# Kernel optimization log

Measured on AMD Instinct MI355X. Metric: run time of the kernel, lower is better.

The kernel has to match this reference:

```python
import jax, jax.numpy as jnp
import numpy as np

B, T, P, E = 4, 16, 256, 768
H, D = 12, 64          # num_heads, kq_size; H*D == E
DFF = 3072
SCALE = D ** (-0.5)
EPS = 1e-5


def _ln(x, g, b):
    m = jnp.mean(x, axis=-1, keepdims=True)
    v = jnp.mean((x - m) ** 2, axis=-1, keepdims=True)
    return (x - m) / jnp.sqrt(v + EPS) * g + b


def setup_inputs() -> dict:
    key = jax.random.key(0)
    ks = jax.random.split(key, 16)
    std = 0.02
    d = {"x": jax.random.normal(ks[0], (B, T, P, E), jnp.float32)}
    # spatial attention params (weights stored as (in, out))
    d["sq_w"] = jax.random.normal(ks[1], (E, H * D), jnp.float32) * std
    d["sk_w"] = jax.random.normal(ks[2], (E, H * D), jnp.float32) * std
    d["sv_w"] = jax.random.normal(ks[3], (E, H * D), jnp.float32) * std
    d["so_w"] = jax.random.normal(ks[4], (H * D, E), jnp.float32) * std
    d["sq_b"] = jnp.zeros((H * D,), jnp.float32)
    d["sk_b"] = jnp.zeros((H * D,), jnp.float32)
    d["sv_b"] = jnp.zeros((H * D,), jnp.float32)
    d["so_b"] = jnp.zeros((E,), jnp.float32)
    d["sg"] = jnp.ones((E,), jnp.float32)
    d["sb"] = jnp.zeros((E,), jnp.float32)
    # temporal attention params
    d["tq_w"] = jax.random.normal(ks[5], (E, H * D), jnp.float32) * std
    d["tk_w"] = jax.random.normal(ks[6], (E, H * D), jnp.float32) * std
    d["tv_w"] = jax.random.normal(ks[7], (E, H * D), jnp.float32) * std
    d["to_w"] = jax.random.normal(ks[8], (H * D, E), jnp.float32) * std
    d["tq_b"] = jnp.zeros((H * D,), jnp.float32)
    d["tk_b"] = jnp.zeros((H * D,), jnp.float32)
    d["tv_b"] = jnp.zeros((H * D,), jnp.float32)
    d["to_b"] = jnp.zeros((E,), jnp.float32)
    d["tg"] = jnp.ones((E,), jnp.float32)
    d["tb"] = jnp.zeros((E,), jnp.float32)
    # FFN + final layernorm
    d["w1"] = jax.random.normal(ks[9], (E, DFF), jnp.float32) * std
    d["b1"] = jnp.zeros((DFF,), jnp.float32)
    d["w2"] = jax.random.normal(ks[10], (DFF, E), jnp.float32) * std
    d["b2"] = jnp.zeros((E,), jnp.float32)
    d["g"] = jnp.ones((E,), jnp.float32)
    d["bb"] = jnp.zeros((E,), jnp.float32)
    return d


def reference(x, sq_w, sq_b, sk_w, sk_b, sv_w, sv_b, so_w, so_b, sg, sb,
              tq_w, tq_b, tk_w, tk_b, tv_w, tv_b, to_w, to_b, tg, tb,
              w1, b1, w2, b2, g, bb):
    b, t, p, e = x.shape

    # ---- Spatial layer: attention over patches P within each frame ----
    q = (x @ sq_w + sq_b).reshape(b, t, p, H, D)
    k = (x @ sk_w + sk_b).reshape(b, t, p, H, D)
    v = (x @ sv_w + sv_b).reshape(b, t, p, H, D)
    attn = jnp.einsum('btphd,btqhd->bthpq', q, k) * SCALE
    attn = jax.nn.softmax(attn, axis=-1)
    out = jnp.einsum('bthpq,btqhd->btphd', attn, v).reshape(b, t, p, H * D)
    out = out @ so_w + so_b
    x = _ln(x + out, sg, sb)

    # ---- Temporal layer: causal attention over frames T per patch ----
    q = (x @ tq_w + tq_b).reshape(b, t, p, H, D)
    k = (x @ tk_w + tk_b).reshape(b, t, p, H, D)
    v = (x @ tv_w + tv_b).reshape(b, t, p, H, D)
    attn = jnp.einsum('btphd,bsphd->bphts', q, k) * SCALE
    causal = jnp.where(jnp.arange(t)[:, None] >= jnp.arange(t)[None, :],
                       jnp.float32(0), -jnp.inf).astype(x.dtype)  # (T, T)
    attn = attn + causal
    attn = jax.nn.softmax(attn, axis=-1)
    out = jnp.einsum('bphts,bsphd->btphd', attn, v).reshape(b, t, p, H * D)
    out = out @ to_w + to_b
    x = _ln(x + out, tg, tb)

    # ---- Feed forward + final layernorm ----
    ff = jax.nn.gelu(x @ w1 + b1, approximate=False) @ w2 + b2
    x = _ln(x + ff, g, bb)
    return x
```

## Files before the change

### kernel.cpp

```cpp
#include <hip/hip_runtime.h>
#include <math.h>

constexpr int cB   = 4;
constexpr int cT   = 16;
constexpr int cP   = 256;
constexpr int cE   = 768;
constexpr int cH   = 12;
constexpr int cD   = 64;
constexpr int cDFF = 3072;
constexpr int NTOK = cB * cT * cP;
constexpr float cSCALE = 0.125f;
constexpr float cEPS = 1e-5f;

typedef __attribute__((ext_vector_type(8))) short short8;
typedef __attribute__((ext_vector_type(4))) float f32x4;
typedef __attribute__((ext_vector_type(8))) unsigned short u16x8;
typedef __attribute__((ext_vector_type(4))) unsigned short u16x4;

#define AS1 __attribute__((address_space(1)))
#define AS3 __attribute__((address_space(3)))

__device__ inline float b2f(unsigned short u) {
    union { unsigned int i; float f; } c; c.i = ((unsigned int)u) << 16; return c.f;
}
__device__ inline unsigned short f2b(float f) {
    union { float f; unsigned int i; } c; c.f = f;
    unsigned int i = c.i;
    unsigned int r = i + 0x7FFFu + ((i >> 16) & 1u);
    return (unsigned short)(r >> 16);
}

__device__ inline void gload16(const unsigned short* g, short* l) {
    __builtin_amdgcn_global_load_lds((AS1 const void*)g, (AS3 void*)l, 16, 0, 0);
}

template<int OUTB, int ACT>
__global__ __launch_bounds__(256) void gemm_mfma_kernel(
    const unsigned short* __restrict__ A,
    const unsigned short* __restrict__ BT,
    const float* __restrict__ bias,
    void* __restrict__ Cout,
    int M, int N, int K)
{
    __shared__ short As[8192];
    __shared__ short Bs[8192];

    const int tid = threadIdx.x;
    const int m0 = blockIdx.y * 128;
    const int n0 = blockIdx.x * 128;
    const int w  = tid >> 6;
    const int l  = tid & 63;
    const int wr = w >> 1, wc = w & 1;
    const int l15 = l & 15, l16 = l >> 4;

    f32x4 acc[4][4];
    #pragma unroll
    for (int i = 0; i < 4; ++i)
        #pragma unroll
        for (int j = 0; j < 4; ++j)
            #pragma unroll
            for (int r = 0; r < 4; ++r) acc[i][j][r] = 0.f;

    const int sr = tid >> 2;
    const int sc = (tid & 3) << 3;
    const unsigned short* ga0 = A  + (size_t)(m0 + sr) * K + sc;
    const unsigned short* ga1 = A  + (size_t)(m0 + 64 + sr) * K + sc;
    const unsigned short* gb0 = BT + (size_t)(n0 + sr) * K + sc;
    const unsigned short* gb1 = BT + (size_t)(n0 + 64 + sr) * K + sc;
    short* lA = As + tid * 8;
    short* lB = Bs + tid * 8;

    const int aoff = (wr * 64 + l15) * 32 + l16 * 8;
    const int boff = (wc * 64 + l15) * 32 + l16 * 8;

    gload16(ga0, lA);
    gload16(ga1, lA + 2048);
    gload16(gb0, lB);
    gload16(gb1, lB + 2048);
    __syncthreads();

    int cur = 0;
    for (int k0 = 0; k0 < K; k0 += 32) {
        if (k0 + 32 < K) {
            const int nb = (cur ^ 1) << 12;
            gload16(ga0 + k0 + 32, lA + nb);
            gload16(ga1 + k0 + 32, lA + nb + 2048);
            gload16(gb0 + k0 + 32, lB + nb);
            gload16(gb1 + k0 + 32, lB + nb + 2048);
        }
        const int cb = cur << 12;
        short8 aF[4], bF[4];
        #pragma unroll
        for (int mf = 0; mf < 4; ++mf)
            aF[mf] = *(const short8*)(As + cb + aoff + mf * 512);
        #pragma unroll
        for (int nf = 0; nf < 4; ++nf)
            bF[nf] = *(const short8*)(Bs + cb + boff + nf * 512);
        #pragma unroll
        for (int mf = 0; mf < 4; ++mf)
            #pragma unroll
            for (int nf = 0; nf < 4; ++nf)
                acc[mf][nf] = __builtin_amdgcn_mfma_f32_16x16x32_bf16(
                    aF[mf], bF[nf], acc[mf][nf], 0, 0, 0);
        __syncthreads();
        cur ^= 1;
    }

    #pragma unroll
    for (int mf = 0; mf < 4; ++mf) {
        #pragma unroll
        for (int nf = 0; nf < 4; ++nf) {
            const int col = n0 + wc * 64 + nf * 16 + l15;
            const float bs = bias[col];
            #pragma unroll
            for (int r = 0; r < 4; ++r) {
                const int row = m0 + wr * 64 + mf * 16 + l16 * 4 + r;
                float v = acc[mf][nf][r] + bs;
                if (ACT) v = 0.5f * v * (1.f + erff(v * 0.70710678118654752f));
                if (OUTB) ((unsigned short*)Cout)[(size_t)row * N + col] = f2b(v);
                else      ((float*)Cout)[(size_t)row * N + col] = v;
            }
        }
    }
}

__global__ __launch_bounds__(256) void transpose_cast_kernel(
    const float* __restrict__ W, unsigned short* __restrict__ WT,
    int K, int N)
{
    __shared__ float t[32][33];
    const int k0 = blockIdx.y * 32;
    const int n0 = blockIdx.x * 32;
    const int tx = threadIdx.x & 31;
    const int ty4 = (threadIdx.x >> 5) << 2;
    #pragma unroll
    for (int i = 0; i < 4; ++i)
        t[ty4 + i][tx] = W[(size_t)(k0 + ty4 + i) * N + n0 + tx];
    __syncthreads();
    #pragma unroll
    for (int i = 0; i < 4; ++i)
        WT[(size_t)(n0 + ty4 + i) * K + k0 + tx] = f2b(t[tx][ty4 + i]);
}

struct TP8 { const float* src[8]; unsigned short* dst[8]; };
__global__ __launch_bounds__(256) void transpose_cast8_kernel(TP8 p)
{
    __shared__ float t[32][33];
    const int z = blockIdx.z;
    const float* W = p.src[z];
    unsigned short* WT = p.dst[z];
    const int k0 = blockIdx.y * 32;
    const int n0 = blockIdx.x * 32;
    const int tx = threadIdx.x & 31;
    const int ty4 = (threadIdx.x >> 5) << 2;
    #pragma unroll
    for (int i = 0; i < 4; ++i)
        t[ty4 + i][tx] = W[(size_t)(k0 + ty4 + i) * cE + n0 + tx];
    __syncthreads();
    #pragma unroll
    for (int i = 0; i < 4; ++i)
        WT[(size_t)(n0 + ty4 + i) * cE + k0 + tx] = f2b(t[tx][ty4 + i]);
}

__global__ __launch_bounds__(256) void cast_bf16_kernel(
    const float* __restrict__ in, unsigned short* __restrict__ out, int n4)
{
    for (int i = blockIdx.x * blockDim.x + threadIdx.x; i < n4;
         i += gridDim.x * blockDim.x) {
        float4 v = ((const float4*)in)[i];
        u16x4 o;
        o[0] = f2b(v.x); o[1] = f2b(v.y); o[2] = f2b(v.z); o[3] = f2b(v.w);
        *(u16x4*)(out + (size_t)i * 4) = o;
    }
}

__global__ __launch_bounds__(256) void residual_ln_kernel(
    const float* __restrict__ X, const float* __restrict__ R,
    const float* __restrict__ gamma, const float* __restrict__ beta,
    float* __restrict__ out, unsigned short* __restrict__ outb)
{
    const int row = blockIdx.x;
    const size_t off = (size_t)row * cE;
    const int tid = threadIdx.x;

    float v[3];
    float s = 0.f, ss = 0.f;
    #pragma unroll
    for (int i = 0; i < 3; ++i) {
        const int e = tid + i * 256;
        const float t = X[off + e] + R[off + e];
        v[i] = t; s += t; ss += t * t;
    }
    #pragma unroll
    for (int o = 32; o > 0; o >>= 1) {
        s  += __shfl_down(s, o);
        ss += __shfl_down(ss, o);
    }
    __shared__ float rs[4], rss[4];
    const int wid = tid >> 6;
    if ((tid & 63) == 0) { rs[wid] = s; rss[wid] = ss; }
    __syncthreads();
    s  = rs[0] + rs[1] + rs[2] + rs[3];
    ss = rss[0] + rss[1] + rss[2] + rss[3];

    const float mean = s * (1.f / cE);
    const float var  = ss * (1.f / cE) - mean * mean;
    const float inv  = rsqrtf(var + cEPS);
    #pragma unroll
    for (int i = 0; i < 3; ++i) {
        const int e = tid + i * 256;
        const float r = (v[i] - mean) * inv * gamma[e] + beta[e];
        out[off + e] = r;
        if (outb) outb[off + e] = f2b(r);
    }
}

__global__ __launch_bounds__(256) void spatial_attn_mfma_kernel(
    const unsigned short* __restrict__ Q, const unsigned short* __restrict__ K,
    const unsigned short* __restrict__ V, unsigned short* __restrict__ O)
{
    __shared__ short Ks[64 * 64];
    __shared__ short Vt[64 * 64];
    __shared__ short Ps[4][64 * 64];

    const int bid = blockIdx.x;
    const int h  = bid % cH;
    const int bt = bid / cH;
    const size_t base = (size_t)bt * cP * cE + h * cD;

    const int tid = threadIdx.x;
    const int w = tid >> 6, l = tid & 63;
    const int l15 = l & 15, l16 = l >> 4;

    short8 qf[4][2];
    #pragma unroll
    for (int mf = 0; mf < 4; ++mf)
        #pragma unroll
        for (int kf = 0; kf < 2; ++kf)
            qf[mf][kf] = *(const short8*)(
                Q + base + (size_t)(w * 64 + mf * 16 + l15) * cE + kf * 32 + l16 * 8);

    f32x4 o[4][4];
    float mrun[4][4], lrun[4][4];
    #pragma unroll
    for (int mf = 0; mf < 4; ++mf)
        #pragma unroll
        for (int j = 0; j < 4; ++j) {
            #pragma unroll
            for (int r = 0; r < 4; ++r) o[mf][j][r] = 0.f;
            mrun[mf][j] = -INFINITY; lrun[mf][j] = 0.f;
        }

    const int krow = w * 8 + (l >> 3);
    const int kc16 = l & 7;
    const int vj  = tid & 31;
    const int vd0 = (tid >> 5) * 8;

    for (int c0 = 0; c0 < cP; c0 += 64) {
        __syncthreads();
        #pragma unroll
        for (int p = 0; p < 2; ++p) {
            const int row = p * 32 + krow;
            gload16(K + base + (size_t)(c0 + row) * cE + ((kc16 ^ (row & 7)) << 3),
                    Ks + row * 64 + kc16 * 8);
        }
        #pragma unroll
        for (int p = 0; p < 2; ++p) {
            const int j = p * 32 + vj;
            short8 vv = *(const short8*)(V + base + (size_t)(c0 + j) * cE + vd0);
            char* vb = (char*)Vt;
            #pragma unroll
            for (int e = 0; e < 8; ++e) {
                const int row = vd0 + e;
                *(short*)(vb + row * 128 + ((2 * j) ^ ((row & 7) << 4))) = vv[e];
            }
        }
        __syncthreads();

        f32x4 s[4][4];
        #pragma unroll
        for (int mf = 0; mf < 4; ++mf)
            #pragma unroll
            for (int nf = 0; nf < 4; ++nf)
                #pragma unroll
                for (int r = 0; r < 4; ++r) s[mf][nf][r] = 0.f;

        #pragma unroll
        for (int nf = 0; nf < 4; ++nf) {
            const int row = nf * 16 + l15;
            const char* kb = (const char*)Ks + row * 128;
            const int sw = (row & 7) << 4;
            short8 k0 = *(const short8*)(kb + ((l16 * 16) ^ sw));
            short8 k1 = *(const short8*)(kb + ((64 + l16 * 16) ^ sw));
            #pragma unroll
            for (int mf = 0; mf < 4; ++mf) {
                s[mf][nf] = __builtin_amdgcn_mfma_f32_16x16x32_bf16(qf[mf][0], k0, s[mf][nf], 0, 0, 0);
                s[mf][nf] = __builtin_amdgcn_mfma_f32_16x16x32_bf16(qf[mf][1], k1, s[mf][nf], 0, 0, 0);
            }
        }

        #pragma unroll
        for (int mf = 0; mf < 4; ++mf)
            #pragma unroll
            for (int nf = 0; nf < 4; ++nf)
                #pragma unroll
                for (int r = 0; r < 4; ++r) s[mf][nf][r] *= cSCALE;

        #pragma unroll
        for (int mf = 0; mf < 4; ++mf) {
            #pragma unroll
            for (int r = 0; r < 4; ++r) {
                float rv = fmaxf(fmaxf(s[mf][0][r], s[mf][1][r]),
                                 fmaxf(s[mf][2][r], s[mf][3][r]));
                rv = fmaxf(rv, __shfl_xor(rv, 1));
                rv = fmaxf(rv, __shfl_xor(rv, 2));
                rv = fmaxf(rv, __shfl_xor(rv, 4));
                rv = fmaxf(rv, __shfl_xor(rv, 8));
                const float mn = fmaxf(mrun[mf][r], rv);
                const float al = __expf(mrun[mf][r] - mn);
                mrun[mf][r] = mn;
                float ps = 0.f;
                #pragma unroll
                for (int nf = 0; nf < 4; ++nf) {
                    const float pe = __expf(s[mf][nf][r] - mn);
                    s[mf][nf][r] = pe;
                    ps += pe;
                }
                ps += __shfl_xor(ps, 1);
                ps += __shfl_xor(ps, 2);
                ps += __shfl_xor(ps, 4);
                ps += __shfl_xor(ps, 8);
                lrun[mf][r] = lrun[mf][r] * al + ps;
                #pragma unroll
                for (int df = 0; df < 4; ++df) o[mf][df][r] *= al;
            }
        }

        char* pw = (char*)&Ps[w][0];
        #pragma unroll
        for (int mf = 0; mf < 4; ++mf)
            #pragma unroll
            for (int nf = 0; nf < 4; ++nf)
                #pragma unroll
                for (int r = 0; r < 4; ++r) {
                    const int row = mf * 16 + l16 * 4 + r;
                    *(short*)(pw + row * 128 + (((nf * 16 + l15) * 2) ^ ((row & 7) << 4))) =
                        (short)f2b(s[mf][nf][r]);
                }

        short8 pa[4][2];
        #pragma unroll
        for (int mf = 0; mf < 4; ++mf) {
            const int prow = mf * 16 + l15;
            const char* pb = (const char*)&Ps[w][0] + prow * 128;
            const int sw = (prow & 7) << 4;
            pa[mf][0] = *(const short8*)(pb + ((l16 * 16) ^ sw));
            pa[mf][1] = *(const short8*)(pb + ((64 + l16 * 16) ^ sw));
        }
        #pragma unroll
        for (int df = 0; df < 4; ++df) {
            const int vrow = df * 16 + l15;
            const char* vbb = (const char*)Vt + vrow * 128;
            const int sw = (vrow & 7) << 4;
            short8 v0 = *(const short8*)(vbb + ((l16 * 16) ^ sw));
            short8 v1 = *(const short8*)(vbb + ((64 + l16 * 16) ^ sw));
            #pragma unroll
            for (int mf = 0; mf < 4; ++mf) {
                o[mf][df] = __builtin_amdgcn_mfma_f32_16x16x32_bf16(pa[mf][0], v0, o[mf][df], 0, 0, 0);
                o[mf][df] = __builtin_amdgcn_mfma_f32_16x16x32_bf16(pa[mf][1], v1, o[mf][df], 0, 0, 0);
            }
        }
    }

    #pragma unroll
    for (int mf = 0; mf < 4; ++mf)
        #pragma unroll
        for (int r = 0; r < 4; ++r) {
            const float inv = 1.f / lrun[mf][r];
            const size_t rowoff = base + (size_t)(w * 64 + mf * 16 + l16 * 4 + r) * cE;
            #pragma unroll
            for (int df = 0; df < 4; ++df)
                O[rowoff + df * 16 + l15] = f2b(o[mf][df][r] * inv);
        }
}

__global__ __launch_bounds__(128) void temporal_attn_kernel(
    const unsigned short* __restrict__ Q, const unsigned short* __restrict__ Kb,
    const unsigned short* __restrict__ V, unsigned short* __restrict__ O)
{
    const int bid = blockIdx.x;
    const int hg  = bid & 1;
    const int bp  = bid >> 1;
    const int p   = bp % cP;
    const int b   = bp / cP;

    __shared__ float Ks[cT][6][cD + 1];
    __shared__ float Vs[cT][6][cD + 1];

    const size_t framestride = (size_t)cP * cE;
    const size_t base0 = ((size_t)(b * cT) * cP + p) * cE + hg * 384;

    for (int li = threadIdx.x; li < cT * 384; li += 128) {
        const int s = li / 384;
        const int r = li % 384;
        const size_t src = base0 + (size_t)s * framestride + r;
        Ks[s][r / 64][r & 63] = b2f(Kb[src]);
        Vs[s][r / 64][r & 63] = b2f(V[src]);
    }
    __syncthreads();
    if (threadIdx.x >= 96) return;

    const int hh = threadIdx.x >> 4;
    const int t  = threadIdx.x & 15;
    const size_t qoff = ((size_t)(b * cT + t) * cP + p) * cE + hg * 384 + hh * cD;

    float q[cD];
    #pragma unroll
    for (int d = 0; d < cD; d += 8) {
        short8 f = *(const short8*)(Q + qoff + d);
        #pragma unroll
        for (int j = 0; j < 8; ++j) q[d + j] = b2f((unsigned short)f[j]);
    }

    float sc[cT];
    float mx = -INFINITY;
    #pragma unroll
    for (int s = 0; s < cT; ++s) {
        float acc = 0.f;
        #pragma unroll
        for (int d = 0; d < cD; ++d) acc = fmaf(q[d], Ks[s][hh][d], acc);
        sc[s] = (s <= t) ? acc * cSCALE : -INFINITY;
        mx = fmaxf(mx, sc[s]);
    }
    float l = 0.f;
    #pragma unroll
    for (int s = 0; s < cT; ++s) {
        const float e_ = __expf(sc[s] - mx);
        sc[s] = e_;
        l += e_;
    }
    float o[cD];
    #pragma unroll
    for (int d = 0; d < cD; ++d) o[d] = 0.f;
    #pragma unroll
    for (int s = 0; s < cT; ++s) {
        const float pj = sc[s];
        #pragma unroll
        for (int d = 0; d < cD; ++d) o[d] = fmaf(pj, Vs[s][hh][d], o[d]);
    }
    const float invl = 1.f / l;
    unsigned short* op = O + qoff;
    #pragma unroll
    for (int d = 0; d < cD; d += 8) {
        u16x8 f;
        #pragma unroll
        for (int j = 0; j < 8; ++j) f[j] = f2b(o[d + j] * invl);
        *(u16x8*)(op + d) = f;
    }
}

extern "C" void kernel_launch(void* const* d_in, const int* in_sizes, int n_in,
                              void* d_out, int out_size, void* d_ws, size_t ws_size,
                              hipStream_t stream)
{
    const float* x    = (const float*)d_in[0];
    const float* sq_w = (const float*)d_in[1];
    const float* sk_w = (const float*)d_in[2];
    const float* sv_w = (const float*)d_in[3];
    const float* so_w = (const float*)d_in[4];
    const float* sq_b = (const float*)d_in[5];
    const float* sk_b = (const float*)d_in[6];
    const float* sv_b = (const float*)d_in[7];
    const float* so_b = (const float*)d_in[8];
    const float* sg   = (const float*)d_in[9];
    const float* sb   = (const float*)d_in[10];
    const float* tq_w = (const float*)d_in[11];
    const float* tk_w = (const float*)d_in[12];
    const float* tv_w = (const float*)d_in[13];
    const float* to_w = (const float*)d_in[14];
    const float* tq_b = (const float*)d_in[15];
    const float* tk_b = (const float*)d_in[16];
    const float* tv_b = (const float*)d_in[17];
    const float* to_b = (const float*)d_in[18];
    const float* tg   = (const float*)d_in[19];
    const float* tb   = (const float*)d_in[20];
    const float* w1   = (const float*)d_in[21];
    const float* b1   = (const float*)d_in[22];
    const float* w2   = (const float*)d_in[23];
    const float* b2   = (const float*)d_in[24];
    const float* g    = (const float*)d_in[25];
    const float* bb   = (const float*)d_in[26];

    const size_t NE = (size_t)NTOK * cE;
    const size_t EE = (size_t)cE * cE;

    float* W0 = (float*)d_ws;
    float* Wp = W0 + NE;
    unsigned short* Xb = (unsigned short*)(Wp + NE);
    unsigned short* Qb = Xb + NE;
    unsigned short* Kbuf = Qb + NE;
    unsigned short* Vb = Kbuf + NE;
    unsigned short* Ob = Vb + NE;
    unsigned short* Hb = Qb;
    unsigned short* WT = Ob + NE;
    unsigned short* sqT = WT;
    unsigned short* skT = sqT + EE;
    unsigned short* svT = skT + EE;
    unsigned short* soT = svT + EE;
    unsigned short* tqT = soT + EE;
    unsigned short* tkT = tqT + EE;
    unsigned short* tvT = tkT + EE;
    unsigned short* toT = tvT + EE;
    unsigned short* w1T = toT + EE;
    unsigned short* w2T = w1T + (size_t)cDFF * cE;

    const dim3 blk(256);
    const dim3 gLN(NTOK);
    const dim3 gProj(cE / 128, NTOK / 128);
    const dim3 gFF1(cDFF / 128, NTOK / 128);

    cast_bf16_kernel<<<dim3(2048), blk, 0, stream>>>(x, Xb, (int)(NE / 4));
    {
        TP8 p;
        p.src[0] = sq_w; p.dst[0] = sqT;
        p.src[1] = sk_w; p.dst[1] = skT;
        p.src[2] = sv_w; p.dst[2] = svT;
        p.src[3] = so_w; p.dst[3] = soT;
        p.src[4] = tq_w; p.dst[4] = tqT;
        p.src[5] = tk_w; p.dst[5] = tkT;
        p.src[6] = tv_w; p.dst[6] = tvT;
        p.src[7] = to_w; p.dst[7] = toT;
        transpose_cast8_kernel<<<dim3(cE / 32, cE / 32, 8), blk, 0, stream>>>(p);
    }
    transpose_cast_kernel<<<dim3(cDFF / 32, cE / 32), blk, 0, stream>>>(w1, w1T, cE, cDFF);
    transpose_cast_kernel<<<dim3(cE / 32, cDFF / 32), blk, 0, stream>>>(w2, w2T, cDFF, cE);

    gemm_mfma_kernel<1,0><<<gProj, blk, 0, stream>>>(Xb, sqT, sq_b, Qb, NTOK, cE, cE);
    gemm_mfma_kernel<1,0><<<gProj, blk, 0, stream>>>(Xb, skT, sk_b, Kbuf, NTOK, cE, cE);
    gemm_mfma_kernel<1,0><<<gProj, blk, 0, stream>>>(Xb, svT, sv_b, Vb, NTOK, cE, cE);
    spatial_attn_mfma_kernel<<<dim3(cB * cT * cH), blk, 0, stream>>>(Qb, Kbuf, Vb, Ob);
    gemm_mfma_kernel<0,0><<<gProj, blk, 0, stream>>>(Ob, soT, so_b, Wp, NTOK, cE, cE);
    residual_ln_kernel<<<gLN, blk, 0, stream>>>(x, Wp, sg, sb, W0, Xb);

    gemm_mfma_kernel<1,0><<<gProj, blk, 0, stream>>>(Xb, tqT, tq_b, Qb, NTOK, cE, cE);
    gemm_mfma_kernel<1,0><<<gProj, blk, 0, stream>>>(Xb, tkT, tk_b, Kbuf, NTOK, cE, cE);
    gemm_mfma_kernel<1,0><<<gProj, blk, 0, stream>>>(Xb, tvT, tv_b, Vb, NTOK, cE, cE);
    temporal_attn_kernel<<<dim3(cB * cP * 2), dim3(128), 0, stream>>>(Qb, Kbuf, Vb, Ob);
    gemm_mfma_kernel<0,0><<<gProj, blk, 0, stream>>>(Ob, toT, to_b, Wp, NTOK, cE, cE);
    residual_ln_kernel<<<gLN, blk, 0, stream>>>(W0, Wp, tg, tb, W0, Xb);

    gemm_mfma_kernel<1,1><<<gFF1, blk, 0, stream>>>(Xb, w1T, b1, Hb, NTOK, cDFF, cE);
    gemm_mfma_kernel<0,0><<<gProj, blk, 0, stream>>>(Hb, w2T, b2, Wp, NTOK, cE, cDFF);
    residual_ln_kernel<<<gLN, blk, 0, stream>>>(W0, Wp, g, bb, (float*)d_out, nullptr);
}
```

Baseline: 785.8 us.

## Replace GEMM with 256x256 swizzled-LDS pipelined kernel and fuse QKV projections

```diff
diff --git a/kernel.cpp b/kernel.cpp
--- a/kernel.cpp
+++ b/kernel.cpp
@@ -34,91 +34,143 @@
     __builtin_amdgcn_global_load_lds((AS1 const void*)g, (AS3 void*)l, 16, 0, 0);
 }
 
-template<int OUTB, int ACT>
-__global__ __launch_bounds__(256) void gemm_mfma_kernel(
+__device__ inline void stage_half(const unsigned short* Xg, int K,
+                                  short* ldsbase, int w, int l) {
+    #pragma unroll
+    for (int j = 0; j < 2; ++j) {
+        const int r = w * 16 + j * 8 + (l >> 3);
+        const int sl = l & 7;
+        gload16(Xg + (size_t)r * K + ((sl ^ (r & 7)) << 3),
+                ldsbase + r * 64 + (sl << 3));
+    }
+}
+
+template<int OUTB, int ACT, int SPLIT3>
+__global__ __launch_bounds__(512, 2) void gemm256_kernel(
     const unsigned short* __restrict__ A,
     const unsigned short* __restrict__ BT,
-    const float* __restrict__ bias,
-    void* __restrict__ Cout,
-    int M, int N, int K)
-{
-    __shared__ short As[8192];
-    __shared__ short Bs[8192];
+    const float* __restrict__ bias0, const float* __restrict__ bias1,
+    const float* __restrict__ bias2,
+    void* __restrict__ C0, void* __restrict__ C1, void* __restrict__ C2,
+    int M, int N, int K, int nbn)
+{
+    __shared__ short As[2 * 256 * 64];
+    __shared__ short Bs[2 * 256 * 64];
 
     const int tid = threadIdx.x;
-    const int m0 = blockIdx.y * 128;
-    const int n0 = blockIdx.x * 128;
-    const int w  = tid >> 6;
-    const int l  = tid & 63;
-    const int wr = w >> 1, wc = w & 1;
+    const int w = tid >> 6, l = tid & 63;
     const int l15 = l & 15, l16 = l >> 4;
-
-    f32x4 acc[4][4];
-    #pragma unroll
-    for (int i = 0; i < 4; ++i)
+    const int wm = w >> 2, wn = w & 3;
+
+    const int nwg = gridDim.x;
+    const int wg = (blockIdx.x & 7) * (nwg >> 3) + (blockIdx.x >> 3);
+    const int bm = wg / nbn, bn = wg % nbn;
+    const int m0 = bm * 256, n0 = bn * 256;
+
+    const unsigned short* pA0 = A + (size_t)m0 * K;
+    const unsigned short* pA1 = A + (size_t)(m0 + 128) * K;
+    const unsigned short* pB0 = BT + (size_t)n0 * K;
+    const unsigned short* pB1 = BT + (size_t)(n0 + 128) * K;
+
+    f32x4 acc[8][4];
+    #pragma unroll
+    for (int i = 0; i < 8; ++i)
         #pragma unroll
         for (int j = 0; j < 4; ++j)
             #pragma unroll
             for (int r = 0; r < 4; ++r) acc[i][j][r] = 0.f;
 
-    const int sr = tid >> 2;
-    const int sc = (tid & 3) << 3;
-    const unsigned short* ga0 = A  + (size_t)(m0 + sr) * K + sc;
-    const unsigned short* ga1 = A  + (size_t)(m0 + 64 + sr) * K + sc;
-    const unsigned short* gb0 = BT + (size_t)(n0 + sr) * K + sc;
-    const unsigned short* gb1 = BT + (size_t)(n0 + 64 + sr) * K + sc;
-    short* lA = As + tid * 8;
-    short* lB = Bs + tid * 8;
-
-    const int aoff = (wr * 64 + l15) * 32 + l16 * 8;
-    const int boff = (wc * 64 + l15) * 32 + l16 * 8;
-
-    gload16(ga0, lA);
-    gload16(ga1, lA + 2048);
-    gload16(gb0, lB);
-    gload16(gb1, lB + 2048);
-    __syncthreads();
-
-    int cur = 0;
-    for (int k0 = 0; k0 < K; k0 += 32) {
-        if (k0 + 32 < K) {
-            const int nb = (cur ^ 1) << 12;
-            gload16(ga0 + k0 + 32, lA + nb);
-            gload16(ga1 + k0 + 32, lA + nb + 2048);
-            gload16(gb0 + k0 + 32, lB + nb);
-            gload16(gb1 + k0 + 32, lB + nb + 2048);
-        }
-        const int cb = cur << 12;
-        short8 aF[4], bF[4];
-        #pragma unroll
-        for (int mf = 0; mf < 4; ++mf)
-            aF[mf] = *(const short8*)(As + cb + aoff + mf * 512);
-        #pragma unroll
-        for (int nf = 0; nf < 4; ++nf)
-            bF[nf] = *(const short8*)(Bs + cb + boff + nf * 512);
-        #pragma unroll
-        for (int mf = 0; mf < 4; ++mf)
-            #pragma unroll
-            for (int nf = 0; nf < 4; ++nf)
-                acc[mf][nf] = __builtin_amdgcn_mfma_f32_16x16x32_bf16(
-                    aF[mf], bF[nf], acc[mf][nf], 0, 0, 0);
-        __syncthreads();
-        cur ^= 1;
-    }
-
-    #pragma unroll
-    for (int mf = 0; mf < 4; ++mf) {
+    stage_half(pA0, K, As, w, l);
+    stage_half(pA1, K, As + 8192, w, l);
+    stage_half(pB0, K, Bs, w, l);
+    stage_half(pB1, K, Bs + 8192, w, l);
+    asm volatile("s_waitcnt vmcnt(0)" ::: "memory");
+    __builtin_amdgcn_s_barrier();
+
+    short8 bF[4][2];
+    const int niter = K >> 7;
+    int k0 = 0;
+    for (int it = 0; it < niter; ++it) {
+        const int kb = k0 + 64;
+        const int kc = (k0 + 128 < K) ? (k0 + 128) : 0;
+        #pragma unroll
+        for (int p = 0; p < 8; ++p) {
+            const int c = p >> 2;
+            const int q = p & 3;
+
+            short8 aF[2][2];
+            if (q == 0) {
+                #pragma unroll
+                for (int nf = 0; nf < 4; ++nf) {
+                    const int rb = wn * 64 + nf * 16 + l15;
+                    const char* pb = (const char*)Bs + c * 32768 + rb * 128;
+                    const int sw = (rb & 7) << 4;
+                    bF[nf][0] = *(const short8*)(pb + ((l16 * 16) ^ sw));
+                    bF[nf][1] = *(const short8*)(pb + ((64 + l16 * 16) ^ sw));
+                }
+            }
+            #pragma unroll
+            for (int mm = 0; mm < 2; ++mm) {
+                const int ra = wm * 128 + (q * 2 + mm) * 16 + l15;
+                const char* pa = (const char*)As + c * 32768 + ra * 128;
+                const int sw = (ra & 7) << 4;
+                aF[mm][0] = *(const short8*)(pa + ((l16 * 16) ^ sw));
+                aF[mm][1] = *(const short8*)(pa + ((64 + l16 * 16) ^ sw));
+            }
+
+            {
+                const int koff = (p < 4) ? kb : kc;
+                short* dst = ((q < 2) ? As : Bs) + ((c ^ 1) * 16384) + ((q & 1) * 8192);
+                const unsigned short* src =
+                    (q == 0 ? pA0 : q == 1 ? pA1 : q == 2 ? pB0 : pB1) + koff;
+                stage_half(src, K, dst, w, l);
+            }
+
+            __builtin_amdgcn_s_barrier();
+            asm volatile("s_waitcnt lgkmcnt(0)" ::: "memory");
+            __builtin_amdgcn_sched_barrier(0);
+            __builtin_amdgcn_s_setprio(1);
+            #pragma unroll
+            for (int kk = 0; kk < 2; ++kk)
+                #pragma unroll
+                for (int nf = 0; nf < 4; ++nf)
+                    #pragma unroll
+                    for (int mm = 0; mm < 2; ++mm)
+                        acc[q * 2 + mm][nf] = __builtin_amdgcn_mfma_f32_16x16x32_bf16(
+                            aF[mm][kk], bF[nf][kk], acc[q * 2 + mm][nf], 0, 0, 0);
+            __builtin_amdgcn_s_setprio(0);
+            __builtin_amdgcn_sched_barrier(0);
+            if (q == 3)
+                asm volatile("s_waitcnt vmcnt(0)" ::: "memory");
+            __builtin_amdgcn_s_barrier();
+        }
+        k0 += 128;
+    }
+
+    #pragma unroll
+    for (int mf = 0; mf < 8; ++mf) {
         #pragma unroll
         for (int nf = 0; nf < 4; ++nf) {
-            const int col = n0 + wc * 64 + nf * 16 + l15;
-            const float bs = bias[col];
+            const int ng = n0 + wn * 64 + nf * 16 + l15;
+            int nl = ng;
+            const float* bp = bias0;
+            void* Cp = C0;
+            int Nout = N;
+            if (SPLIT3) {
+                const int which = ng / 768;
+                nl = ng - which * 768;
+                bp = (which == 0) ? bias0 : (which == 1) ? bias1 : bias2;
+                Cp = (which == 0) ? C0 : (which == 1) ? C1 : C2;
+                Nout = 768;
+            }
+            const float bs = bp[nl];
             #pragma unroll
             for (int r = 0; r < 4; ++r) {
-                const int row = m0 + wr * 64 + mf * 16 + l16 * 4 + r;
+                const int row = m0 + wm * 128 + mf * 16 + l16 * 4 + r;
                 float v = acc[mf][nf][r] + bs;
                 if (ACT) v = 0.5f * v * (1.f + erff(v * 0.70710678118654752f));
-                if (OUTB) ((unsigned short*)Cout)[(size_t)row * N + col] = f2b(v);
-                else      ((float*)Cout)[(size_t)row * N + col] = v;
+                if (OUTB) ((unsigned short*)Cp)[(size_t)row * Nout + nl] = f2b(v);
+                else      ((float*)Cp)[(size_t)row * Nout + nl] = v;
             }
         }
     }
@@ -515,9 +567,11 @@
     unsigned short* w2T = w1T + (size_t)cDFF * cE;
 
     const dim3 blk(256);
+    const dim3 blk512(512);
     const dim3 gLN(NTOK);
-    const dim3 gProj(cE / 128, NTOK / 128);
-    const dim3 gFF1(cDFF / 128, NTOK / 128);
+    const dim3 gQKV(576);
+    const dim3 gOUT(192);
+    const dim3 gFF1(768);
 
     cast_bf16_kernel<<<dim3(2048), blk, 0, stream>>>(x, Xb, (int)(NE / 4));
     {
@@ -535,21 +589,23 @@
     transpose_cast_kernel<<<dim3(cDFF / 32, cE / 32), blk, 0, stream>>>(w1, w1T, cE, cDFF);
     transpose_cast_kernel<<<dim3(cE / 32, cDFF / 32), blk, 0, stream>>>(w2, w2T, cDFF, cE);
 
-    gemm_mfma_kernel<1,0><<<gProj, blk, 0, stream>>>(Xb, sqT, sq_b, Qb, NTOK, cE, cE);
-    gemm_mfma_kernel<1,0><<<gProj, blk, 0, stream>>>(Xb, skT, sk_b, Kbuf, NTOK, cE, cE);
-    gemm_mfma_kernel<1,0><<<gProj, blk, 0, stream>>>(Xb, svT, sv_b, Vb, NTOK, cE, cE);
+    gemm256_kernel<1,0,1><<<gQKV, blk512, 0, stream>>>(
+        Xb, sqT, sq_b, sk_b, sv_b, Qb, Kbuf, Vb, NTOK, 2304, cE, 9);
     spatial_attn_mfma_kernel<<<dim3(cB * cT * cH), blk, 0, stream>>>(Qb, Kbuf, Vb, Ob);
-    gemm_mfma_kernel<0,0><<<gProj, blk, 0, stream>>>(Ob, soT, so_b, Wp, NTOK, cE, cE);
+    gemm256_kernel<0,0,0><<<gOUT, blk512, 0, stream>>>(
+        Ob, soT, so_b, nullptr, nullptr, Wp, nullptr, nullptr, NTOK, cE, cE, 3);
     residual_ln_kernel<<<gLN, blk, 0, stream>>>(x, Wp, sg, sb, W0, Xb);
 
-    gemm_mfma_kernel<1,0><<<gProj, blk, 0, stream>>>(Xb, tqT, tq_b, Qb, NTOK, cE, cE);
-    gemm_mfma_kernel<1,0><<<gProj, blk, 0, stream>>>(Xb, tkT, tk_b, Kbuf, NTOK, cE, cE);
-    gemm_mfma_kernel<1,0><<<gProj, blk, 0, stream>>>(Xb, tvT, tv_b, Vb, NTOK, cE, cE);
+    gemm256_kernel<1,0,1><<<gQKV, blk512, 0, stream>>>(
+        Xb, tqT, tq_b, tk_b, tv_b, Qb, Kbuf, Vb, NTOK, 2304, cE, 9);
     temporal_attn_kernel<<<dim3(cB * cP * 2), dim3(128), 0, stream>>>(Qb, Kbuf, Vb, Ob);
-    gemm_mfma_kernel<0,0><<<gProj, blk, 0, stream>>>(Ob, toT, to_b, Wp, NTOK, cE, cE);
+    gemm256_kernel<0,0,0><<<gOUT, blk512, 0, stream>>>(
+        Ob, toT, to_b, nullptr, nullptr, Wp, nullptr, nullptr, NTOK, cE, cE, 3);
     residual_ln_kernel<<<gLN, blk, 0, stream>>>(W0, Wp, tg, tb, W0, Xb);
 
-    gemm_mfma_kernel<1,1><<<gFF1, blk, 0, stream>>>(Xb, w1T, b1, Hb, NTOK, cDFF, cE);
-    gemm_mfma_kernel<0,0><<<gProj, blk, 0, stream>>>(Hb, w2T, b2, Wp, NTOK, cE, cDFF);
+    gemm256_kernel<1,1,0><<<gFF1, blk512, 0, stream>>>(
+        Xb, w1T, b1, nullptr, nullptr, Hb, nullptr, nullptr, NTOK, cDFF, cE, 12);
+    gemm256_kernel<0,0,0><<<gOUT, blk512, 0, stream>>>(
+        Hb, w2T, b2, nullptr, nullptr, Wp, nullptr, nullptr, NTOK, cE, cDFF, 3);
     residual_ln_kernel<<<gLN, blk, 0, stream>>>(W0, Wp, g, bb, (float*)d_out, nullptr);
 }
```

Result: faster. 755.5 us (-3.9%).
